# Performance work log

Hardware: AMD Instinct MI355X
Metric: run time of the kernel (lower is better)

## Reference

```python
import jax, jax.numpy as jnp
import numpy as np

L, D, H, DFF = 12, 768, 12, 3072
DH = D // H
EPS = 1e-5


def _layer_norm(x, g, b):
    # manual LN as in source: biased variance, eps inside sqrt
    mean = jnp.mean(x, axis=-1, keepdims=True)
    var = jnp.mean((x - mean) ** 2, axis=-1, keepdims=True)
    return g * (x - mean) / jnp.sqrt(var + EPS) + b


def setup_inputs() -> dict:
    key = jax.random.key(0)
    ks = jax.random.split(key, 10)
    x = jax.random.normal(ks[0], (8, 512, D), dtype=jnp.float32)
    mask = jnp.zeros((8, 1, 1, 512), dtype=jnp.float32)
    s = 0.02
    Wq = jax.random.normal(ks[1], (L, D, D), jnp.float32) * s
    Wk = jax.random.normal(ks[2], (L, D, D), jnp.float32) * s
    Wv = jax.random.normal(ks[3], (L, D, D), jnp.float32) * s
    Wo = jax.random.normal(ks[4], (L, D, D), jnp.float32) * s
    W1 = jax.random.normal(ks[5], (L, DFF, D), jnp.float32) * s
    W2 = jax.random.normal(ks[6], (L, D, DFF), jnp.float32) * s
    z = lambda *sh: jnp.zeros(sh, jnp.float32)
    o = lambda *sh: jnp.ones(sh, jnp.float32)
    return {
        'x': x, 'mask': mask,
        'Wq': Wq, 'bq': z(L, D), 'Wk': Wk, 'bk': z(L, D), 'Wv': Wv, 'bv': z(L, D),
        'Wo': Wo, 'bo': z(L, D), 'g1': o(L, D), 'b1': z(L, D),
        'W1': W1, 'bf1': z(L, DFF), 'W2': W2, 'bf2': z(L, D),
        'g2': o(L, D), 'b2': z(L, D),
    }


def reference(x, mask, Wq, bq, Wk, bk, Wv, bv, Wo, bo, g1, b1, W1, bf1, W2, bf2, g2, b2):
    B, S, _ = x.shape
    scale = 1.0 / jnp.sqrt(jnp.float32(DH))

    def layer(h, p):
        wq, pq, wk, pk, wv, pv, wo, po, gg1, bb1, w1, pf1, w2, pf2, gg2, bb2 = p
        # Dense: x @ W^T + b
        q = (h @ wq.T + pq).reshape(B, S, H, DH).transpose(0, 2, 1, 3)  # [B,H,S,dh]
        k = (h @ wk.T + pk).reshape(B, S, H, DH).transpose(0, 2, 1, 3)
        v = (h @ wv.T + pv).reshape(B, S, H, DH).transpose(0, 2, 1, 3)
        scores = jnp.einsum('bhqd,bhkd->bhqk', q, k) * scale
        scores = scores + mask * -1e9
        attn = jax.nn.softmax(scores, axis=-1)
        ctx = jnp.einsum('bhqk,bhkd->bhqd', attn, v)
        ctx = ctx.transpose(0, 2, 1, 3).reshape(B, S, D)
        a = _layer_norm(h + (ctx @ wo.T + po), gg1, bb1)
        ffn = jnp.maximum(a @ w1.T + pf1, 0.0) @ w2.T + pf2
        out = _layer_norm(a + ffn, gg2, bb2)
        return out, None

    params = (Wq, bq, Wk, bk, Wv, bv, Wo, bo, g1, b1, W1, bf1, W2, bf2, g2, b2)
    out, _ = jax.lax.scan(layer, x, params)
    return out
```

## Files before the change

kernel.cpp:

```cpp
#include <hip/hip_runtime.h>
#include <hip/hip_bf16.h>
#include <stdint.h>

#define DDIM 768
#define NH 12
#define DHD 64
#define DFF 3072
#define NLAYER 12
#define SEQ 512
#define NB 8
#define ROWS (NB*SEQ)

typedef __attribute__((ext_vector_type(4))) float f32x4;
typedef __attribute__((ext_vector_type(8))) short short8;

#define S_BARRIER()  asm volatile("s_barrier" ::: "memory")
#define WAIT_LGKM0() asm volatile("s_waitcnt lgkmcnt(0)" ::: "memory")
#define WAIT_VM0()   asm volatile("s_waitcnt vmcnt(0)" ::: "memory")
#define WAIT_VM3()   asm volatile("s_waitcnt vmcnt(3)" ::: "memory")
#define WAIT_VM4()   asm volatile("s_waitcnt vmcnt(4)" ::: "memory")

static __device__ __forceinline__ short bf16r(float f) {
  union { float f; uint32_t u; } a; a.f = f;
  uint32_t u = a.u;
  u += 0x7FFFu + ((u >> 16) & 1u);
  return (short)(u >> 16);
}

static __device__ __forceinline__ float bf2f(short s) {
  union { uint32_t u; float f; } c;
  c.u = ((uint32_t)(uint16_t)s) << 16;
  return c.f;
}

static __device__ __forceinline__ f32x4 mfma_bf16(short8 a, short8 b, f32x4 c) {
  return __builtin_amdgcn_mfma_f32_16x16x32_bf16(a, b, c, 0, 0, 0);
}

static __device__ __forceinline__ void gload16(const void* g, void* l) {
  __builtin_amdgcn_global_load_lds(
      (__attribute__((address_space(1))) void*)(void*)(uintptr_t)g,
      (__attribute__((address_space(3))) void*)l,
      16, 0, 0);
}

struct WCvt {
  const float* src[4];
  short* dst[4];
  int n8[4];
};

__global__ void wconv_kernel(WCvt wc) {
  const int m = blockIdx.y;
  const float* __restrict__ src = wc.src[m];
  short* __restrict__ dst = wc.dst[m];
  const int n8 = wc.n8[m];
  for (int i = blockIdx.x * 256 + threadIdx.x; i < n8; i += gridDim.x * 256) {
    f32x4 a = *(const f32x4*)(src + (size_t)i * 8);
    f32x4 b = *(const f32x4*)(src + (size_t)i * 8 + 4);
    short8 o;
    o[0] = bf16r(a[0]); o[1] = bf16r(a[1]); o[2] = bf16r(a[2]); o[3] = bf16r(a[3]);
    o[4] = bf16r(b[0]); o[5] = bf16r(b[1]); o[6] = bf16r(b[2]); o[7] = bf16r(b[3]);
    *(short8*)(dst + (size_t)i * 8) = o;
  }
}

struct GemmB {
  const short* W0; const short* W1; const short* W2;
  const float* b0; const float* b1; const float* b2;
  void* o0; void* o1; void* o2;
};

template<int OUTMODE, int BM>
__launch_bounds__(256, 3)
__global__ void gemm_bt(const short* __restrict__ A, GemmB gb, int M, int N, int K) {
  constexpr int MF  = BM / 32;
  constexpr int ISS = BM / 64;

  const int z = blockIdx.z;
  const short* W    = (z == 0) ? gb.W0 : ((z == 1) ? gb.W1 : gb.W2);
  const float* bias = (z == 0) ? gb.b0 : ((z == 1) ? gb.b1 : gb.b2);
  void* outp        = (z == 0) ? gb.o0 : ((z == 1) ? gb.o1 : gb.o2);

  __shared__ __align__(16) short As[2][BM * 32];
  __shared__ __align__(16) short Bs[2][128 * 32];

  const int tid  = threadIdx.x;
  const int lane = tid & 63;
  const int wid  = tid >> 6;
  const int l16  = lane & 15;
  const int kg   = lane >> 4;
  const int wr   = wid >> 1;
  const int wc   = wid & 1;
  const int m0   = blockIdx.x * BM;
  const int n0   = blockIdx.y * 128;

  const f32x4 zero = {0.f, 0.f, 0.f, 0.f};
  f32x4 acc[MF][4];
  #pragma unroll
  for (int i = 0; i < MF; i++)
    #pragma unroll
    for (int j = 0; j < 4; j++) acc[i][j] = zero;

  const int lrow = lane >> 2;
  const int lcol = (lane & 3) * 8;
  const short* Ag = A + (size_t)(m0 + wid * (BM / 4) + lrow) * K + lcol;
  const short* Wg = W + (size_t)(n0 + wid * 32 + lrow) * K + lcol;

  auto stage = [&](int buf, int k0) {
    #pragma unroll
    for (int j = 0; j < ISS; j++)
      gload16(Ag + k0 + (size_t)(j * 16) * K, &As[buf][(wid * (BM / 4) + j * 16) * 32]);
    #pragma unroll
    for (int j = 0; j < 2; j++)
      gload16(Wg + k0 + (size_t)(j * 16) * K, &Bs[buf][(wid * 32 + j * 16) * 32]);
  };

  const int nsteps = K >> 5;
  stage(0, 0);
  stage(1, 32);
  if (ISS == 2) { WAIT_VM4(); } else { WAIT_VM3(); }
  S_BARRIER();

  for (int t = 0; t < nsteps; ++t) {
    const int cur = t & 1;
    short8 af[MF], bfr[4];
    #pragma unroll
    for (int i = 0; i < MF; i++)
      af[i] = *(const short8*)&As[cur][(wr * (BM / 2) + i * 16 + l16) * 32 + kg * 8];
    #pragma unroll
    for (int j = 0; j < 4; j++)
      bfr[j] = *(const short8*)&Bs[cur][(wc * 64 + j * 16 + l16) * 32 + kg * 8];
    WAIT_LGKM0();
    S_BARRIER();

    const bool pf = (t + 2 < nsteps);
    if (pf) stage(cur, (t + 2) << 5);
    __builtin_amdgcn_sched_barrier(0);
    #pragma unroll
    for (int i = 0; i < MF; i++)
      #pragma unroll
      for (int j = 0; j < 4; j++)
        acc[i][j] = mfma_bf16(af[i], bfr[j], acc[i][j]);
    __builtin_amdgcn_sched_barrier(0);

    if (pf) { if (ISS == 2) { WAIT_VM4(); } else { WAIT_VM3(); } }
    else    { WAIT_VM0(); }
    S_BARRIER();
  }

  float* outf = (float*)outp;
  short* outb = (short*)outp;
  #pragma unroll
  for (int j = 0; j < 4; j++) {
    const int col = n0 + wc * 64 + j * 16 + l16;
    const float bv = bias[col];
    #pragma unroll
    for (int i = 0; i < MF; i++) {
      const int row0 = m0 + wr * (BM / 2) + i * 16 + kg * 4;
      #pragma unroll
      for (int e = 0; e < 4; e++) {
        float v = acc[i][j][e] + bv;
        if (OUTMODE == 2) v = fmaxf(v, 0.0f);
        const size_t off = (size_t)(row0 + e) * N + col;
        if (OUTMODE == 0) outf[off] = v;
        else              outb[off] = bf16r(v);
      }
    }
  }
}

__launch_bounds__(256, 2)
__global__ void attn_kernel(const short* __restrict__ Qg, const short* __restrict__ Kg,
                            const short* __restrict__ Vg, const float* __restrict__ mask,
                            short* __restrict__ ctx) {
  __shared__ __align__(16) short Vt[64 * 512];

  const int bh = blockIdx.x;
  const int b = bh / NH;
  const int h = bh % NH;
  const int tid  = threadIdx.x;
  const int lane = tid & 63;
  const int wid  = tid >> 6;
  const int l16  = lane & 15;
  const int kg   = lane >> 4;

  const short* Qb = Qg + (size_t)b * SEQ * DDIM + h * DHD;
  const short* Kb = Kg + (size_t)b * SEQ * DDIM + h * DHD;
  const short* Vb = Vg + (size_t)b * SEQ * DDIM + h * DHD;

  for (int c = tid; c < SEQ * 8; c += 256) {
    const int kv = c >> 3;
    const int d0 = (c & 7) * 8;
    short8 v = *(const short8*)(Vb + (size_t)kv * DDIM + d0);
    #pragma unroll
    for (int j = 0; j < 8; j++)
      Vt[(d0 + j) * 512 + (kv ^ ((j & 3) << 3))] = v[j];
  }
  __syncthreads();

  const int q0 = blockIdx.y * 128 + wid * 32;

  short8 qf[2][2];
  #pragma unroll
  for (int rt = 0; rt < 2; rt++)
    #pragma unroll
    for (int dh = 0; dh < 2; dh++)
      qf[rt][dh] = *(const short8*)(Qb + (size_t)(q0 + rt * 16 + l16) * DDIM + dh * 32 + kg * 8);

  float mrun[2] = {-1e30f, -1e30f};
  float lrun[2] = {0.0f, 0.0f};
  const f32x4 zero = {0.f, 0.f, 0.f, 0.f};
  f32x4 oacc[2][4];
  #pragma unroll
  for (int rt = 0; rt < 2; rt++)
    #pragma unroll
    for (int dt = 0; dt < 4; dt++) oacc[rt][dt] = zero;

  const float* maskb = mask + (size_t)b * SEQ;

  for (int kv0 = 0; kv0 < SEQ; kv0 += 32) {
    short8 kf[2][2];
    #pragma unroll
    for (int kvh = 0; kvh < 2; kvh++)
      #pragma unroll
      for (int dh = 0; dh < 2; dh++)
        kf[kvh][dh] = *(const short8*)(Kb + (size_t)(kv0 + kvh * 16 + l16) * DDIM + dh * 32 + kg * 8);

    short8 vf[4];
    #pragma unroll
    for (int dt = 0; dt < 4; dt++) {
      const int d = dt * 16 + l16;
      vf[dt] = *(const short8*)&Vt[d * 512 + ((kv0 + kg * 8) ^ ((d & 3) << 3))];
    }

    const f32x4 mq0 = *(const f32x4*)(maskb + kv0 + kg * 4);
    const f32x4 mq1 = *(const f32x4*)(maskb + kv0 + 16 + kg * 4);

    #pragma unroll
    for (int rt = 0; rt < 2; rt++) {
      f32x4 s0 = zero, s1 = zero;
      s0 = mfma_bf16(kf[0][0], qf[rt][0], s0);
      s0 = mfma_bf16(kf[0][1], qf[rt][1], s0);
      s1 = mfma_bf16(kf[1][0], qf[rt][0], s1);
      s1 = mfma_bf16(kf[1][1], qf[rt][1], s1);

      float p[8];
      #pragma unroll
      for (int e = 0; e < 4; e++) {
        p[e]     = s0[e] * 0.125f + mq0[e] * (-1e9f);
        p[e + 4] = s1[e] * 0.125f + mq1[e] * (-1e9f);
      }
      float mt = p[0];
      #pragma unroll
      for (int e = 1; e < 8; e++) mt = fmaxf(mt, p[e]);
      mt = fmaxf(mt, __shfl_xor(mt, 16, 64));
      mt = fmaxf(mt, __shfl_xor(mt, 32, 64));
      const float mnew = fmaxf(mrun[rt], mt);
      const float corr = __expf(mrun[rt] - mnew);
      float ts = 0.0f;
      #pragma unroll
      for (int e = 0; e < 8; e++) { p[e] = __expf(p[e] - mnew); ts += p[e]; }
      ts += __shfl_xor(ts, 16, 64);
      ts += __shfl_xor(ts, 32, 64);
      lrun[rt] = lrun[rt] * corr + ts;
      mrun[rt] = mnew;

      const int P0 = (int)(((uint32_t)(uint16_t)bf16r(p[1]) << 16) | (uint16_t)bf16r(p[0]));
      const int P1 = (int)(((uint32_t)(uint16_t)bf16r(p[3]) << 16) | (uint16_t)bf16r(p[2]));
      const int P2 = (int)(((uint32_t)(uint16_t)bf16r(p[5]) << 16) | (uint16_t)bf16r(p[4]));
      const int P3 = (int)(((uint32_t)(uint16_t)bf16r(p[7]) << 16) | (uint16_t)bf16r(p[6]));
      const int sl0 = (((2 * kg) & 3) << 4) + l16;
      const int sl1 = (((2 * kg + 1) & 3) << 4) + l16;
      const int x0 = __shfl(P0, sl0, 64), y0 = __shfl(P2, sl0, 64);
      const int x1 = __shfl(P1, sl0, 64), y1 = __shfl(P3, sl0, 64);
      const int x2 = __shfl(P0, sl1, 64), y2 = __shfl(P2, sl1, 64);
      const int x3 = __shfl(P1, sl1, 64), y3 = __shfl(P3, sl1, 64);
      union { int w[4]; short8 v; } pa;
      const bool hi = (kg >= 2);
      pa.w[0] = hi ? y0 : x0;
      pa.w[1] = hi ? y1 : x1;
      pa.w[2] = hi ? y2 : x2;
      pa.w[3] = hi ? y3 : x3;

      const float c0 = __shfl(corr, kg * 4 + 0, 64);
      const float c1 = __shfl(corr, kg * 4 + 1, 64);
      const float c2 = __shfl(corr, kg * 4 + 2, 64);
      const float c3 = __shfl(corr, kg * 4 + 3, 64);

      #pragma unroll
      for (int dt = 0; dt < 4; dt++) {
        f32x4 o = oacc[rt][dt];
        o[0] *= c0; o[1] *= c1; o[2] *= c2; o[3] *= c3;
        oacc[rt][dt] = mfma_bf16(pa.v, vf[dt], o);
      }
    }
  }

  short* cb = ctx + (size_t)b * SEQ * DDIM + h * DHD;
  #pragma unroll
  for (int rt = 0; rt < 2; rt++) {
    const float li = 1.0f / lrun[rt];
    const float l0 = __shfl(li, kg * 4 + 0, 64);
    const float l1 = __shfl(li, kg * 4 + 1, 64);
    const float l2 = __shfl(li, kg * 4 + 2, 64);
    const float l3 = __shfl(li, kg * 4 + 3, 64);
    #pragma unroll
    for (int dt = 0; dt < 4; dt++) {
      const f32x4 o = oacc[rt][dt];
      const int col = dt * 16 + l16;
      const size_t base = (size_t)(q0 + rt * 16 + kg * 4) * DDIM + col;
      cb[base + 0 * DDIM] = bf16r(o[0] * l0);
      cb[base + 1 * DDIM] = bf16r(o[1] * l1);
      cb[base + 2 * DDIM] = bf16r(o[2] * l2);
      cb[base + 3 * DDIM] = bf16r(o[3] * l3);
    }
  }
}

template<int PBF16>
__launch_bounds__(256, 4)
__global__ void ln_kernel(const float* __restrict__ resid, const void* __restrict__ projv,
                          const float* __restrict__ gw, const float* __restrict__ bw,
                          float* __restrict__ outf, short* __restrict__ outb) {
  const int lane = threadIdx.x & 63;
  const int wid  = threadIdx.x >> 6;
  const int row  = blockIdx.x * 4 + wid;
  const float* rp = resid + (size_t)row * DDIM;
  float v[12];
  float s = 0.0f;
  #pragma unroll
  for (int c = 0; c < 12; c++) {
    float pv;
    if (PBF16) pv = bf2f(((const short*)projv)[(size_t)row * DDIM + c * 64 + lane]);
    else       pv = ((const float*)projv)[(size_t)row * DDIM + c * 64 + lane];
    v[c] = rp[c * 64 + lane] + pv;
    s += v[c];
  }
  #pragma unroll
  for (int o = 1; o < 64; o <<= 1) s += __shfl_xor(s, o, 64);
  const float mean = s * (1.0f / 768.0f);
  float q = 0.0f;
  #pragma unroll
  for (int c = 0; c < 12; c++) { const float d = v[c] - mean; q += d * d; }
  #pragma unroll
  for (int o = 1; o < 64; o <<= 1) q += __shfl_xor(q, o, 64);
  const float inv = 1.0f / sqrtf(q * (1.0f / 768.0f) + 1e-5f);
  #pragma unroll
  for (int c = 0; c < 12; c++) {
    const int idx = c * 64 + lane;
    const float y = gw[idx] * (v[c] - mean) * inv + bw[idx];
    outf[(size_t)row * DDIM + idx] = y;
    outb[(size_t)row * DDIM + idx] = bf16r(y);
  }
}

extern "C" void kernel_launch(void* const* d_in, const int* in_sizes, int n_in,
                              void* d_out, int out_size, void* d_ws, size_t ws_size,
                              hipStream_t stream) {
  const float* x    = (const float*)d_in[0];
  const float* mask = (const float*)d_in[1];
  const float* Wq   = (const float*)d_in[2];
  const float* bq   = (const float*)d_in[3];
  const float* Wk   = (const float*)d_in[4];
  const float* bk   = (const float*)d_in[5];
  const float* Wv   = (const float*)d_in[6];
  const float* bv   = (const float*)d_in[7];
  const float* Wo   = (const float*)d_in[8];
  const float* bo   = (const float*)d_in[9];
  const float* g1   = (const float*)d_in[10];
  const float* b1   = (const float*)d_in[11];
  const float* W1   = (const float*)d_in[12];
  const float* bf1  = (const float*)d_in[13];
  const float* W2   = (const float*)d_in[14];
  const float* bf2  = (const float*)d_in[15];
  const float* g2   = (const float*)d_in[16];
  const float* b2   = (const float*)d_in[17];

  const size_t SD  = (size_t)ROWS * DDIM;
  const size_t WDD = (size_t)DDIM * DDIM;
  const size_t WFD = (size_t)DFF * DDIM;

  char* ws = (char*)d_ws;
  float* H0   = (float*)ws;  ws += SD * 4;
  short* Bbuf = (short*)ws;  ws += SD * 2;
  short* R1   = (short*)ws;  ws += (size_t)ROWS * DFF * 2;
  short* WB   = (short*)ws;

  short* Qb = R1;
  short* Kb = R1 + SD;
  short* Vb = R1 + 2 * SD;
  short* Cb = R1 + 3 * SD;
  float* Pf = (float*)R1;

  {
    WCvt c{};
    c.src[0] = x; c.dst[0] = Bbuf; c.n8[0] = (int)(SD / 8);
    wconv_kernel<<<dim3(1536, 1), 256, 0, stream>>>(c);
  }

  for (int l = 0; l < NLAYER; l++) {
    {
      WCvt c{};
      c.src[0] = Wq + l * WDD; c.dst[0] = WB;           c.n8[0] = (int)(WDD / 8);
      c.src[1] = Wk + l * WDD; c.dst[1] = WB + WDD;     c.n8[1] = (int)(WDD / 8);
      c.src[2] = Wv + l * WDD; c.dst[2] = WB + 2 * WDD; c.n8[2] = (int)(WDD / 8);
      c.src[3] = Wo + l * WDD; c.dst[3] = WB + 3 * WDD; c.n8[3] = (int)(WDD / 8);
      wconv_kernel<<<dim3(288, 4), 256, 0, stream>>>(c);
    }

    {
      GemmB g{};
      g.W0 = WB;           g.b0 = bq + l * DDIM; g.o0 = Qb;
      g.W1 = WB + WDD;     g.b1 = bk + l * DDIM; g.o1 = Kb;
      g.W2 = WB + 2 * WDD; g.b2 = bv + l * DDIM; g.o2 = Vb;
      gemm_bt<1, 128><<<dim3(32, 6, 3), 256, 0, stream>>>(Bbuf, g, ROWS, DDIM, DDIM);
    }

    attn_kernel<<<dim3(NB * NH, 4), 256, 0, stream>>>(Qb, Kb, Vb, mask, Cb);

    {
      GemmB g{};
      g.W0 = WB + 3 * WDD; g.b0 = bo + l * DDIM; g.o0 = Pf;
      gemm_bt<0, 64><<<dim3(64, 6, 1), 256, 0, stream>>>(Cb, g, ROWS, DDIM, DDIM);
    }

    {
      WCvt c{};
      c.src[0] = W1 + l * WFD; c.dst[0] = WB;       c.n8[0] = (int)(WFD / 8);
      c.src[1] = W2 + l * WFD; c.dst[1] = WB + WFD; c.n8[1] = (int)(WFD / 8);
      wconv_kernel<<<dim3(1152, 2), 256, 0, stream>>>(c);
    }

    ln_kernel<0><<<dim3(ROWS / 4), 256, 0, stream>>>(l ? H0 : x, Pf,
                                                     g1 + l * DDIM, b1 + l * DDIM,
                                                     H0, Bbuf);

    {
      GemmB g{};
      g.W0 = WB; g.b0 = bf1 + l * DFF; g.o0 = R1;
      gemm_bt<2, 128><<<dim3(32, 24, 1), 256, 0, stream>>>(Bbuf, g, ROWS, DFF, DDIM);
    }

    {
      GemmB g{};
      g.W0 = WB + WFD; g.b0 = bf2 + l * DDIM; g.o0 = Bbuf;
      gemm_bt<1, 64><<<dim3(64, 6, 1), 256, 0, stream>>>(R1, g, ROWS, DDIM, DFF);
    }

    ln_kernel<1><<<dim3(ROWS / 4), 256, 0, stream>>>(H0, Bbuf,
                                                     g2 + l * DDIM, b2 + l * DDIM,
                                                     (l == NLAYER - 1) ? (float*)d_out : H0,
                                                     Bbuf);
  }
}
```

Before: 2.099 ms.

## Convert all layer weights upfront and fuse QKV into one concatenated GEMM

All twelve layers' weights are converted to bf16 in a single kernel before the layer loop, along with the input, replacing the per-layer conversion launches. Q, K and V weights sit contiguously, so one GEMM with N=2304 and concatenated biases writes an interleaved QKV buffer, which attention now reads with a 2304-element row stride. Separate workspace buffers are used instead of aliasing, and the GEMM launch bound is raised to 4 blocks per CU. This cuts launch count and per-layer conversion traffic, at the cost of a larger workspace and one big upfront conversion pass.

```diff
diff --git a/kernel.cpp b/kernel.cpp
--- a/kernel.cpp
+++ b/kernel.cpp
@@ -10,6 +10,7 @@
 #define SEQ 512
 #define NB 8
 #define ROWS (NB*SEQ)
+#define QS   2304
 
 typedef __attribute__((ext_vector_type(4))) float f32x4;
 typedef __attribute__((ext_vector_type(8))) short short8;
@@ -44,43 +45,67 @@
       16, 0, 0);
 }
 
-struct WCvt {
-  const float* src[4];
-  short* dst[4];
-  int n8[4];
+#define WDD    589824
+#define WFD    2359296
+#define WLAYER (4*WDD + 2*WFD)
+
+struct WAll {
+  const float* src[7];
+  short* wb;
+  short* xb;
 };
 
-__global__ void wconv_kernel(WCvt wc) {
-  const int m = blockIdx.y;
-  const float* __restrict__ src = wc.src[m];
-  short* __restrict__ dst = wc.dst[m];
-  const int n8 = wc.n8[m];
-  for (int i = blockIdx.x * 256 + threadIdx.x; i < n8; i += gridDim.x * 256) {
+__global__ void wconv_all_kernel(WAll wa) {
+  const int y = blockIdx.y;
+  const float* __restrict__ src = wa.src[y];
+  if (y == 6) {
+    short* __restrict__ dst = wa.xb;
+    const int n8 = (ROWS * DDIM) / 8;
+    for (int i = blockIdx.x * 256 + threadIdx.x; i < n8; i += gridDim.x * 256) {
+      f32x4 a = *(const f32x4*)(src + (size_t)i * 8);
+      f32x4 b = *(const f32x4*)(src + (size_t)i * 8 + 4);
+      short8 o;
+      o[0] = bf16r(a[0]); o[1] = bf16r(a[1]); o[2] = bf16r(a[2]); o[3] = bf16r(a[3]);
+      o[4] = bf16r(b[0]); o[5] = bf16r(b[1]); o[6] = bf16r(b[2]); o[7] = bf16r(b[3]);
+      *(short8*)(dst + (size_t)i * 8) = o;
+    }
+    return;
+  }
+  const int perL8  = (y < 4 ? WDD : WFD) / 8;
+  const int dstOff = (y < 4) ? y * WDD : 4 * WDD + (y - 4) * WFD;
+  const int tot    = NLAYER * perL8;
+  for (int i = blockIdx.x * 256 + threadIdx.x; i < tot; i += gridDim.x * 256) {
+    const int l = i / perL8;
+    const int r = i - l * perL8;
     f32x4 a = *(const f32x4*)(src + (size_t)i * 8);
     f32x4 b = *(const f32x4*)(src + (size_t)i * 8 + 4);
     short8 o;
     o[0] = bf16r(a[0]); o[1] = bf16r(a[1]); o[2] = bf16r(a[2]); o[3] = bf16r(a[3]);
     o[4] = bf16r(b[0]); o[5] = bf16r(b[1]); o[6] = bf16r(b[2]); o[7] = bf16r(b[3]);
-    *(short8*)(dst + (size_t)i * 8) = o;
-  }
-}
-
-struct GemmB {
-  const short* W0; const short* W1; const short* W2;
-  const float* b0; const float* b1; const float* b2;
-  void* o0; void* o1; void* o2;
-};
+    *(short8*)(wa.wb + (size_t)l * WLAYER + dstOff + (size_t)r * 8) = o;
+  }
+}
+
+__global__ void bcat_kernel(const float* __restrict__ bq, const float* __restrict__ bk,
+                            const float* __restrict__ bv, float* __restrict__ out) {
+  const int idx = blockIdx.x * 256 + threadIdx.x;
+  if (idx >= NLAYER * QS) return;
+  const int l = idx / QS;
+  const int j = idx - l * QS;
+  float v;
+  if (j < DDIM)            v = bq[l * DDIM + j];
+  else if (j < 2 * DDIM)   v = bk[l * DDIM + j - DDIM];
+  else                     v = bv[l * DDIM + j - 2 * DDIM];
+  out[idx] = v;
+}
 
 template<int OUTMODE, int BM>
-__launch_bounds__(256, 3)
-__global__ void gemm_bt(const short* __restrict__ A, GemmB gb, int M, int N, int K) {
+__launch_bounds__(256, 4)
+__global__ void gemm_bt(const short* __restrict__ A, const short* __restrict__ W,
+                        const float* __restrict__ bias, void* __restrict__ outp,
+                        int M, int N, int K) {
   constexpr int MF  = BM / 32;
   constexpr int ISS = BM / 64;
-
-  const int z = blockIdx.z;
-  const short* W    = (z == 0) ? gb.W0 : ((z == 1) ? gb.W1 : gb.W2);
-  const float* bias = (z == 0) ? gb.b0 : ((z == 1) ? gb.b1 : gb.b2);
-  void* outp        = (z == 0) ? gb.o0 : ((z == 1) ? gb.o1 : gb.o2);
 
   __shared__ __align__(16) short As[2][BM * 32];
   __shared__ __align__(16) short Bs[2][128 * 32];
@@ -171,8 +196,7 @@
 }
 
 __launch_bounds__(256, 2)
-__global__ void attn_kernel(const short* __restrict__ Qg, const short* __restrict__ Kg,
-                            const short* __restrict__ Vg, const float* __restrict__ mask,
+__global__ void attn_kernel(const short* __restrict__ QKV, const float* __restrict__ mask,
                             short* __restrict__ ctx) {
   __shared__ __align__(16) short Vt[64 * 512];
 
@@ -185,14 +209,14 @@
   const int l16  = lane & 15;
   const int kg   = lane >> 4;
 
-  const short* Qb = Qg + (size_t)b * SEQ * DDIM + h * DHD;
-  const short* Kb = Kg + (size_t)b * SEQ * DDIM + h * DHD;
-  const short* Vb = Vg + (size_t)b * SEQ * DDIM + h * DHD;
+  const short* Qb = QKV + (size_t)b * SEQ * QS + h * DHD;
+  const short* Kb = Qb + DDIM;
+  const short* Vb = Qb + 2 * DDIM;
 
   for (int c = tid; c < SEQ * 8; c += 256) {
     const int kv = c >> 3;
     const int d0 = (c & 7) * 8;
-    short8 v = *(const short8*)(Vb + (size_t)kv * DDIM + d0);
+    short8 v = *(const short8*)(Vb + (size_t)kv * QS + d0);
     #pragma unroll
     for (int j = 0; j < 8; j++)
       Vt[(d0 + j) * 512 + (kv ^ ((j & 3) << 3))] = v[j];
@@ -206,7 +230,7 @@
   for (int rt = 0; rt < 2; rt++)
     #pragma unroll
     for (int dh = 0; dh < 2; dh++)
-      qf[rt][dh] = *(const short8*)(Qb + (size_t)(q0 + rt * 16 + l16) * DDIM + dh * 32 + kg * 8);
+      qf[rt][dh] = *(const short8*)(Qb + (size_t)(q0 + rt * 16 + l16) * QS + dh * 32 + kg * 8);
 
   float mrun[2] = {-1e30f, -1e30f};
   float lrun[2] = {0.0f, 0.0f};
@@ -225,7 +249,7 @@
     for (int kvh = 0; kvh < 2; kvh++)
       #pragma unroll
       for (int dh = 0; dh < 2; dh++)
-        kf[kvh][dh] = *(const short8*)(Kb + (size_t)(kv0 + kvh * 16 + l16) * DDIM + dh * 32 + kg * 8);
+        kf[kvh][dh] = *(const short8*)(Kb + (size_t)(kv0 + kvh * 16 + l16) * QS + dh * 32 + kg * 8);
 
     short8 vf[4];
     #pragma unroll
@@ -377,79 +401,50 @@
   const float* g2   = (const float*)d_in[16];
   const float* b2   = (const float*)d_in[17];
 
-  const size_t SD  = (size_t)ROWS * DDIM;
-  const size_t WDD = (size_t)DDIM * DDIM;
-  const size_t WFD = (size_t)DFF * DDIM;
+  const size_t SD = (size_t)ROWS * DDIM;
 
   char* ws = (char*)d_ws;
   float* H0   = (float*)ws;  ws += SD * 4;
   short* Bbuf = (short*)ws;  ws += SD * 2;
-  short* R1   = (short*)ws;  ws += (size_t)ROWS * DFF * 2;
+  short* QKVb = (short*)ws;  ws += (size_t)ROWS * QS * 2;
+  short* Cb   = (short*)ws;  ws += SD * 2;
+  float* Pf   = (float*)ws;  ws += SD * 4;
+  short* F1   = (short*)ws;  ws += (size_t)ROWS * DFF * 2;
+  float* Bqkv = (float*)ws;  ws += (size_t)NLAYER * QS * 4;
   short* WB   = (short*)ws;
 
-  short* Qb = R1;
-  short* Kb = R1 + SD;
-  short* Vb = R1 + 2 * SD;
-  short* Cb = R1 + 3 * SD;
-  float* Pf = (float*)R1;
-
   {
-    WCvt c{};
-    c.src[0] = x; c.dst[0] = Bbuf; c.n8[0] = (int)(SD / 8);
-    wconv_kernel<<<dim3(1536, 1), 256, 0, stream>>>(c);
+    WAll wa{};
+    wa.src[0] = Wq; wa.src[1] = Wk; wa.src[2] = Wv; wa.src[3] = Wo;
+    wa.src[4] = W1; wa.src[5] = W2; wa.src[6] = x;
+    wa.wb = WB; wa.xb = Bbuf;
+    wconv_all_kernel<<<dim3(1024, 7), 256, 0, stream>>>(wa);
+    bcat_kernel<<<dim3((NLAYER * QS + 255) / 256), 256, 0, stream>>>(bq, bk, bv, Bqkv);
   }
 
   for (int l = 0; l < NLAYER; l++) {
-    {
-      WCvt c{};
-      c.src[0] = Wq + l * WDD; c.dst[0] = WB;           c.n8[0] = (int)(WDD / 8);
-      c.src[1] = Wk + l * WDD; c.dst[1] = WB + WDD;     c.n8[1] = (int)(WDD / 8);
-      c.src[2] = Wv + l * WDD; c.dst[2] = WB + 2 * WDD; c.n8[2] = (int)(WDD / 8);
-      c.src[3] = Wo + l * WDD; c.dst[3] = WB + 3 * WDD; c.n8[3] = (int)(WDD / 8);
-      wconv_kernel<<<dim3(288, 4), 256, 0, stream>>>(c);
-    }
-
-    {
-      GemmB g{};
-      g.W0 = WB;           g.b0 = bq + l * DDIM; g.o0 = Qb;
-      g.W1 = WB + WDD;     g.b1 = bk + l * DDIM; g.o1 = Kb;
-      g.W2 = WB + 2 * WDD; g.b2 = bv + l * DDIM; g.o2 = Vb;
-      gemm_bt<1, 128><<<dim3(32, 6, 3), 256, 0, stream>>>(Bbuf, g, ROWS, DDIM, DDIM);
-    }
-
-    attn_kernel<<<dim3(NB * NH, 4), 256, 0, stream>>>(Qb, Kb, Vb, mask, Cb);
-
-    {
-      GemmB g{};
-      g.W0 = WB + 3 * WDD; g.b0 = bo + l * DDIM; g.o0 = Pf;
-      gemm_bt<0, 64><<<dim3(64, 6, 1), 256, 0, stream>>>(Cb, g, ROWS, DDIM, DDIM);
-    }
-
-    {
-      WCvt c{};
-      c.src[0] = W1 + l * WFD; c.dst[0] = WB;       c.n8[0] = (int)(WFD / 8);
-      c.src[1] = W2 + l * WFD; c.dst[1] = WB + WFD; c.n8[1] = (int)(WFD / 8);
-      wconv_kernel<<<dim3(1152, 2), 256, 0, stream>>>(c);
-    }
+    const short* WL = WB + (size_t)l * WLAYER;
+
+    gemm_bt<1, 128><<<dim3(32, 18), 256, 0, stream>>>(
+        Bbuf, WL, Bqkv + (size_t)l * QS, QKVb, ROWS, QS, DDIM);
+
+    attn_kernel<<<dim3(NB * NH, 4), 256, 0, stream>>>(QKVb, mask, Cb);
+
+    gemm_bt<0, 64><<<dim3(64, 6), 256, 0, stream>>>(
+        Cb, WL + 3 * WDD, bo + (size_t)l * DDIM, Pf, ROWS, DDIM, DDIM);
 
     ln_kernel<0><<<dim3(ROWS / 4), 256, 0, stream>>>(l ? H0 : x, Pf,
-                                                     g1 + l * DDIM, b1 + l * DDIM,
+                                                     g1 + (size_t)l * DDIM, b1 + (size_t)l * DDIM,
                                                      H0, Bbuf);
 
-    {
-      GemmB g{};
-      g.W0 = WB; g.b0 = bf1 + l * DFF; g.o0 = R1;
-      gemm_bt<2, 128><<<dim3(32, 24, 1), 256, 0, stream>>>(Bbuf, g, ROWS, DFF, DDIM);
-    }
-
-    {
-      GemmB g{};
-      g.W0 = WB + WFD; g.b0 = bf2 + l * DDIM; g.o0 = Bbuf;
-      gemm_bt<1, 64><<<dim3(64, 6, 1), 256, 0, stream>>>(R1, g, ROWS, DDIM, DFF);
-    }
+    gemm_bt<2, 128><<<dim3(32, 24), 256, 0, stream>>>(
+        Bbuf, WL + 4 * WDD, bf1 + (size_t)l * DFF, F1, ROWS, DFF, DDIM);
+
+    gemm_bt<1, 64><<<dim3(64, 6), 256, 0, stream>>>(
+        F1, WL + 4 * WDD + WFD, bf2 + (size_t)l * DDIM, Bbuf, ROWS, DDIM, DFF);
 
     ln_kernel<1><<<dim3(ROWS / 4), 256, 0, stream>>>(H0, Bbuf,
-                                                     g2 + l * DDIM, b2 + l * DDIM,
+                                                     g2 + (size_t)l * DDIM, b2 + (size_t)l * DDIM,
                                                      (l == NLAYER - 1) ? (float*)d_out : H0,
                                                      Bbuf);
   }
```

Measured after the change: 2.238 ms. 1.07x slower.

## Fuse next-layer weight bf16 conversion into FFN1 GEMM with double-buffered weights

Applied to the files above, without the earlier changes.

Removes the two per-layer weight-conversion launches. The FFN1 GEMM grid gets 9 extra rows of blocks (288 blocks) that convert the next layer's attention and FFN weights into a second, ping-pong weight buffer while the GEMM tiles run. This saves launches and lets the memory-bound conversion overlap the compute-bound GEMM. The cost is a double workspace for bf16 weights and possible contention between the converter blocks and the GEMM blocks for bandwidth and CU slots.

```diff
diff --git a/kernel.cpp b/kernel.cpp
--- a/kernel.cpp
+++ b/kernel.cpp
@@ -20,6 +20,9 @@
 #define WAIT_VM3()   asm volatile("s_waitcnt vmcnt(3)" ::: "memory")
 #define WAIT_VM4()   asm volatile("s_waitcnt vmcnt(4)" ::: "memory")
 
+#define WDD    589824
+#define WFD    2359296
+
 static __device__ __forceinline__ short bf16r(float f) {
   union { float f; uint32_t u; } a; a.f = f;
   uint32_t u = a.u;
@@ -44,6 +47,16 @@
       16, 0, 0);
 }
 
+static __device__ __forceinline__ void cvt8(const float* __restrict__ s,
+                                            short* __restrict__ d) {
+  f32x4 a = *(const f32x4*)(s);
+  f32x4 b = *(const f32x4*)(s + 4);
+  short8 o;
+  o[0] = bf16r(a[0]); o[1] = bf16r(a[1]); o[2] = bf16r(a[2]); o[3] = bf16r(a[3]);
+  o[4] = bf16r(b[0]); o[5] = bf16r(b[1]); o[6] = bf16r(b[2]); o[7] = bf16r(b[3]);
+  *(short8*)d = o;
+}
+
 struct WCvt {
   const float* src[4];
   short* dst[4];
@@ -55,14 +68,8 @@
   const float* __restrict__ src = wc.src[m];
   short* __restrict__ dst = wc.dst[m];
   const int n8 = wc.n8[m];
-  for (int i = blockIdx.x * 256 + threadIdx.x; i < n8; i += gridDim.x * 256) {
-    f32x4 a = *(const f32x4*)(src + (size_t)i * 8);
-    f32x4 b = *(const f32x4*)(src + (size_t)i * 8 + 4);
-    short8 o;
-    o[0] = bf16r(a[0]); o[1] = bf16r(a[1]); o[2] = bf16r(a[2]); o[3] = bf16r(a[3]);
-    o[4] = bf16r(b[0]); o[5] = bf16r(b[1]); o[6] = bf16r(b[2]); o[7] = bf16r(b[3]);
-    *(short8*)(dst + (size_t)i * 8) = o;
-  }
+  for (int i = blockIdx.x * 256 + threadIdx.x; i < n8; i += gridDim.x * 256)
+    cvt8(src + (size_t)i * 8, dst + (size_t)i * 8);
 }
 
 struct GemmB {
@@ -71,11 +78,36 @@
   void* o0; void* o1; void* o2;
 };
 
-template<int OUTMODE, int BM>
+struct ConvNext {
+  const float* srcA[4];
+  const float* srcB[2];
+  short* dstA;
+  short* dstB;
+};
+
+template<int OUTMODE, int BM, int FUSECONV>
 __launch_bounds__(256, 3)
-__global__ void gemm_bt(const short* __restrict__ A, GemmB gb, int M, int N, int K) {
+__global__ void gemm_bt(const short* __restrict__ A, GemmB gb, ConvNext cn,
+                        int M, int N, int K, int nby) {
   constexpr int MF  = BM / 32;
   constexpr int ISS = BM / 64;
+
+  if (FUSECONV && (int)blockIdx.y >= nby) {
+    const int cid = ((int)blockIdx.y - nby) * (int)gridDim.x + (int)blockIdx.x;
+    for (int i = cid * 256 + (int)threadIdx.x; i < 884736; i += 288 * 256) {
+      if (i < 294912) {
+        const int m = i / 73728;
+        const int r = i - m * 73728;
+        cvt8(cn.srcA[m] + (size_t)r * 8, cn.dstA + (size_t)m * WDD + (size_t)r * 8);
+      } else {
+        const int c2 = i - 294912;
+        const int m = c2 / 294912;
+        const int r = c2 - m * 294912;
+        cvt8(cn.srcB[m] + (size_t)r * 8, cn.dstB + (size_t)m * WFD + (size_t)r * 8);
+      }
+    }
+    return;
+  }
 
   const int z = blockIdx.z;
   const short* W    = (z == 0) ? gb.W0 : ((z == 1) ? gb.W1 : gb.W2);
@@ -377,15 +409,18 @@
   const float* g2   = (const float*)d_in[16];
   const float* b2   = (const float*)d_in[17];
 
-  const size_t SD  = (size_t)ROWS * DDIM;
-  const size_t WDD = (size_t)DDIM * DDIM;
-  const size_t WFD = (size_t)DFF * DDIM;
+  const size_t SD = (size_t)ROWS * DDIM;
 
   char* ws = (char*)d_ws;
-  float* H0   = (float*)ws;  ws += SD * 4;
-  short* Bbuf = (short*)ws;  ws += SD * 2;
-  short* R1   = (short*)ws;  ws += (size_t)ROWS * DFF * 2;
-  short* WB   = (short*)ws;
+  float* H0     = (float*)ws;  ws += SD * 4;
+  short* Bbuf   = (short*)ws;  ws += SD * 2;
+  short* R1     = (short*)ws;  ws += (size_t)ROWS * DFF * 2;
+  short* WBa[2];
+  WBa[0] = (short*)ws;  ws += (size_t)4 * WDD * 2;
+  WBa[1] = (short*)ws;  ws += (size_t)4 * WDD * 2;
+  short* WBb[2];
+  WBb[0] = (short*)ws;  ws += (size_t)2 * WFD * 2;
+  WBb[1] = (short*)ws;  ws += (size_t)2 * WFD * 2;
 
   short* Qb = R1;
   short* Kb = R1 + SD;
@@ -398,58 +433,76 @@
     c.src[0] = x; c.dst[0] = Bbuf; c.n8[0] = (int)(SD / 8);
     wconv_kernel<<<dim3(1536, 1), 256, 0, stream>>>(c);
   }
+  {
+    WCvt c{};
+    c.src[0] = Wq; c.dst[0] = WBa[0];           c.n8[0] = (int)(WDD / 8);
+    c.src[1] = Wk; c.dst[1] = WBa[0] + WDD;     c.n8[1] = (int)(WDD / 8);
+    c.src[2] = Wv; c.dst[2] = WBa[0] + 2 * WDD; c.n8[2] = (int)(WDD / 8);
+    c.src[3] = Wo; c.dst[3] = WBa[0] + 3 * WDD; c.n8[3] = (int)(WDD / 8);
+    wconv_kernel<<<dim3(288, 4), 256, 0, stream>>>(c);
+  }
+  {
+    WCvt c{};
+    c.src[0] = W1; c.dst[0] = WBb[0];       c.n8[0] = (int)(WFD / 8);
+    c.src[1] = W2; c.dst[1] = WBb[0] + WFD; c.n8[1] = (int)(WFD / 8);
+    wconv_kernel<<<dim3(1152, 2), 256, 0, stream>>>(c);
+  }
+
+  const ConvNext cnDummy{};
 
   for (int l = 0; l < NLAYER; l++) {
-    {
-      WCvt c{};
-      c.src[0] = Wq + l * WDD; c.dst[0] = WB;           c.n8[0] = (int)(WDD / 8);
-      c.src[1] = Wk + l * WDD; c.dst[1] = WB + WDD;     c.n8[1] = (int)(WDD / 8);
-      c.src[2] = Wv + l * WDD; c.dst[2] = WB + 2 * WDD; c.n8[2] = (int)(WDD / 8);
-      c.src[3] = Wo + l * WDD; c.dst[3] = WB + 3 * WDD; c.n8[3] = (int)(WDD / 8);
-      wconv_kernel<<<dim3(288, 4), 256, 0, stream>>>(c);
-    }
+    const short* WA = WBa[l & 1];
+    const short* WF = WBb[l & 1];
 
     {
       GemmB g{};
-      g.W0 = WB;           g.b0 = bq + l * DDIM; g.o0 = Qb;
-      g.W1 = WB + WDD;     g.b1 = bk + l * DDIM; g.o1 = Kb;
-      g.W2 = WB + 2 * WDD; g.b2 = bv + l * DDIM; g.o2 = Vb;
-      gemm_bt<1, 128><<<dim3(32, 6, 3), 256, 0, stream>>>(Bbuf, g, ROWS, DDIM, DDIM);
+      g.W0 = WA;           g.b0 = bq + (size_t)l * DDIM; g.o0 = Qb;
+      g.W1 = WA + WDD;     g.b1 = bk + (size_t)l * DDIM; g.o1 = Kb;
+      g.W2 = WA + 2 * WDD; g.b2 = bv + (size_t)l * DDIM; g.o2 = Vb;
+      gemm_bt<1, 128, 0><<<dim3(32, 6, 3), 256, 0, stream>>>(
+          Bbuf, g, cnDummy, ROWS, DDIM, DDIM, 6);
     }
 
     attn_kernel<<<dim3(NB * NH, 4), 256, 0, stream>>>(Qb, Kb, Vb, mask, Cb);
 
     {
       GemmB g{};
-      g.W0 = WB + 3 * WDD; g.b0 = bo + l * DDIM; g.o0 = Pf;
-      gemm_bt<0, 64><<<dim3(64, 6, 1), 256, 0, stream>>>(Cb, g, ROWS, DDIM, DDIM);
-    }
-
-    {
-      WCvt c{};
-      c.src[0] = W1 + l * WFD; c.dst[0] = WB;       c.n8[0] = (int)(WFD / 8);
-      c.src[1] = W2 + l * WFD; c.dst[1] = WB + WFD; c.n8[1] = (int)(WFD / 8);
-      wconv_kernel<<<dim3(1152, 2), 256, 0, stream>>>(c);
+      g.W0 = WA + 3 * WDD; g.b0 = bo + (size_t)l * DDIM; g.o0 = Pf;
+      gemm_bt<0, 64, 0><<<dim3(64, 6, 1), 256, 0, stream>>>(
+          Cb, g, cnDummy, ROWS, DDIM, DDIM, 6);
     }
 
     ln_kernel<0><<<dim3(ROWS / 4), 256, 0, stream>>>(l ? H0 : x, Pf,
-                                                     g1 + l * DDIM, b1 + l * DDIM,
+                                                     g1 + (size_t)l * DDIM, b1 + (size_t)l * DDIM,
                                                      H0, Bbuf);
 
     {
       GemmB g{};
-      g.W0 = WB; g.b0 = bf1 + l * DFF; g.o0 = R1;
-      gemm_bt<2, 128><<<dim3(32, 24, 1), 256, 0, stream>>>(Bbuf, g, ROWS, DFF, DDIM);
+      g.W0 = WF; g.b0 = bf1 + (size_t)l * DFF; g.o0 = R1;
+      const int nl = (l + 1 < NLAYER) ? (l + 1) : l;
+      ConvNext cn{};
+      cn.srcA[0] = Wq + (size_t)nl * WDD;
+      cn.srcA[1] = Wk + (size_t)nl * WDD;
+      cn.srcA[2] = Wv + (size_t)nl * WDD;
+      cn.srcA[3] = Wo + (size_t)nl * WDD;
+      cn.srcB[0] = W1 + (size_t)nl * WFD;
+      cn.srcB[1] = W2 + (size_t)nl * WFD;
+      cn.dstA = WBa[(l + 1) & 1];
+      cn.dstB = WBb[(l + 1) & 1];
+      const int gy = (l + 1 < NLAYER) ? 33 : 24;
+      gemm_bt<2, 128, 1><<<dim3(32, gy, 1), 256, 0, stream>>>(
+          Bbuf, g, cn, ROWS, DFF, DDIM, 24);
     }
 
     {
       GemmB g{};
-      g.W0 = WB + WFD; g.b0 = bf2 + l * DDIM; g.o0 = Bbuf;
-      gemm_bt<1, 64><<<dim3(64, 6, 1), 256, 0, stream>>>(R1, g, ROWS, DDIM, DFF);
+      g.W0 = WF + WFD; g.b0 = bf2 + (size_t)l * DDIM; g.o0 = Bbuf;
+      gemm_bt<1, 64, 0><<<dim3(64, 6, 1), 256, 0, stream>>>(
+          R1, g, cnDummy, ROWS, DDIM, DFF, 6);
     }
 
     ln_kernel<1><<<dim3(ROWS / 4), 256, 0, stream>>>(H0, Bbuf,
-                                                     g2 + l * DDIM, b2 + l * DDIM,
+                                                     g2 + (size_t)l * DDIM, b2 + (size_t)l * DDIM,
                                                      (l == NLAYER - 1) ? (float*)d_out : H0,
                                                      Bbuf);
   }
```

Measured after the change: 2.154 ms. +2.6%, slower.

## Split-K the N=768 projection GEMMs and fuse partial reduction into LayerNorm

Applied to the files above, without the earlier changes.

The Wo and W2 GEMMs (N=768, grid 64x6=384 blocks) now run as 2-way split-K, doubling the block count to raise occupancy across the CUs. Each half writes fp32 partial sums to separate workspace buffers, and a new LayerNorm kernel adds residual, both partials and bias before normalising. The cost is extra fp32 partial traffic (two 12 MB buffers written and read) and a larger workspace. The FFN2 output also changes from bf16 to fp32 partials, which slightly alters precision.

```diff
diff --git a/kernel.cpp b/kernel.cpp
--- a/kernel.cpp
+++ b/kernel.cpp
@@ -19,6 +19,9 @@
 #define WAIT_VM0()   asm volatile("s_waitcnt vmcnt(0)" ::: "memory")
 #define WAIT_VM3()   asm volatile("s_waitcnt vmcnt(3)" ::: "memory")
 #define WAIT_VM4()   asm volatile("s_waitcnt vmcnt(4)" ::: "memory")
+
+#define WDD    589824
+#define WFD    2359296
 
 static __device__ __forceinline__ short bf16r(float f) {
   union { float f; uint32_t u; } a; a.f = f;
@@ -71,16 +74,26 @@
   void* o0; void* o1; void* o2;
 };
 
-template<int OUTMODE, int BM>
+template<int OUTMODE, int BM, int SPLITK>
 __launch_bounds__(256, 3)
-__global__ void gemm_bt(const short* __restrict__ A, GemmB gb, int M, int N, int K) {
+__global__ void gemm_bt(const short* __restrict__ A, GemmB gb,
+                        int M, int N, int Kstride, int Klen) {
   constexpr int MF  = BM / 32;
   constexpr int ISS = BM / 64;
 
   const int z = blockIdx.z;
-  const short* W    = (z == 0) ? gb.W0 : ((z == 1) ? gb.W1 : gb.W2);
-  const float* bias = (z == 0) ? gb.b0 : ((z == 1) ? gb.b1 : gb.b2);
-  void* outp        = (z == 0) ? gb.o0 : ((z == 1) ? gb.o1 : gb.o2);
+  const short* W;
+  const float* bias;
+  void* outp;
+  if (SPLITK) {
+    W    = gb.W0 + (size_t)z * Klen;
+    bias = gb.b0;
+    outp = (z == 0) ? gb.o0 : gb.o1;
+  } else {
+    W    = (z == 0) ? gb.W0 : ((z == 1) ? gb.W1 : gb.W2);
+    bias = (z == 0) ? gb.b0 : ((z == 1) ? gb.b1 : gb.b2);
+    outp = (z == 0) ? gb.o0 : ((z == 1) ? gb.o1 : gb.o2);
+  }
 
   __shared__ __align__(16) short As[2][BM * 32];
   __shared__ __align__(16) short Bs[2][128 * 32];
@@ -104,19 +117,20 @@
 
   const int lrow = lane >> 2;
   const int lcol = (lane & 3) * 8;
-  const short* Ag = A + (size_t)(m0 + wid * (BM / 4) + lrow) * K + lcol;
-  const short* Wg = W + (size_t)(n0 + wid * 32 + lrow) * K + lcol;
+  const short* Ag = A + (size_t)(m0 + wid * (BM / 4) + lrow) * Kstride + lcol
+                      + (SPLITK ? (size_t)z * Klen : 0);
+  const short* Wg = W + (size_t)(n0 + wid * 32 + lrow) * Kstride + lcol;
 
   auto stage = [&](int buf, int k0) {
     #pragma unroll
     for (int j = 0; j < ISS; j++)
-      gload16(Ag + k0 + (size_t)(j * 16) * K, &As[buf][(wid * (BM / 4) + j * 16) * 32]);
+      gload16(Ag + k0 + (size_t)(j * 16) * Kstride, &As[buf][(wid * (BM / 4) + j * 16) * 32]);
     #pragma unroll
     for (int j = 0; j < 2; j++)
-      gload16(Wg + k0 + (size_t)(j * 16) * K, &Bs[buf][(wid * 32 + j * 16) * 32]);
+      gload16(Wg + k0 + (size_t)(j * 16) * Kstride, &Bs[buf][(wid * 32 + j * 16) * 32]);
   };
 
-  const int nsteps = K >> 5;
+  const int nsteps = Klen >> 5;
   stage(0, 0);
   stage(1, 32);
   if (ISS == 2) { WAIT_VM4(); } else { WAIT_VM3(); }
@@ -154,7 +168,7 @@
   #pragma unroll
   for (int j = 0; j < 4; j++) {
     const int col = n0 + wc * 64 + j * 16 + l16;
-    const float bv = bias[col];
+    const float bv = (OUTMODE == 3) ? 0.0f : bias[col];
     #pragma unroll
     for (int i = 0; i < MF; i++) {
       const int row0 = m0 + wr * (BM / 2) + i * 16 + kg * 4;
@@ -163,7 +177,7 @@
         float v = acc[i][j][e] + bv;
         if (OUTMODE == 2) v = fmaxf(v, 0.0f);
         const size_t off = (size_t)(row0 + e) * N + col;
-        if (OUTMODE == 0) outf[off] = v;
+        if (OUTMODE == 3) outf[off] = v;
         else              outb[off] = bf16r(v);
       }
     }
@@ -318,23 +332,24 @@
   }
 }
 
-template<int PBF16>
 __launch_bounds__(256, 4)
-__global__ void ln_kernel(const float* __restrict__ resid, const void* __restrict__ projv,
-                          const float* __restrict__ gw, const float* __restrict__ bw,
-                          float* __restrict__ outf, short* __restrict__ outb) {
+__global__ void ln_red_kernel(const float* __restrict__ resid,
+                              const float* __restrict__ p0,
+                              const float* __restrict__ p1,
+                              const float* __restrict__ pb,
+                              const float* __restrict__ gw,
+                              const float* __restrict__ bw,
+                              float* __restrict__ outf, short* __restrict__ outb) {
   const int lane = threadIdx.x & 63;
   const int wid  = threadIdx.x >> 6;
   const int row  = blockIdx.x * 4 + wid;
-  const float* rp = resid + (size_t)row * DDIM;
+  const size_t base = (size_t)row * DDIM;
   float v[12];
   float s = 0.0f;
   #pragma unroll
   for (int c = 0; c < 12; c++) {
-    float pv;
-    if (PBF16) pv = bf2f(((const short*)projv)[(size_t)row * DDIM + c * 64 + lane]);
-    else       pv = ((const float*)projv)[(size_t)row * DDIM + c * 64 + lane];
-    v[c] = rp[c * 64 + lane] + pv;
+    const int idx = c * 64 + lane;
+    v[c] = resid[base + idx] + p0[base + idx] + p1[base + idx] + pb[idx];
     s += v[c];
   }
   #pragma unroll
@@ -350,8 +365,8 @@
   for (int c = 0; c < 12; c++) {
     const int idx = c * 64 + lane;
     const float y = gw[idx] * (v[c] - mean) * inv + bw[idx];
-    outf[(size_t)row * DDIM + idx] = y;
-    outb[(size_t)row * DDIM + idx] = bf16r(y);
+    outf[base + idx] = y;
+    outb[base + idx] = bf16r(y);
   }
 }
 
@@ -377,21 +392,20 @@
   const float* g2   = (const float*)d_in[16];
   const float* b2   = (const float*)d_in[17];
 
-  const size_t SD  = (size_t)ROWS * DDIM;
-  const size_t WDD = (size_t)DDIM * DDIM;
-  const size_t WFD = (size_t)DFF * DDIM;
+  const size_t SD = (size_t)ROWS * DDIM;
 
   char* ws = (char*)d_ws;
   float* H0   = (float*)ws;  ws += SD * 4;
   short* Bbuf = (short*)ws;  ws += SD * 2;
   short* R1   = (short*)ws;  ws += (size_t)ROWS * DFF * 2;
-  short* WB   = (short*)ws;
+  short* WB   = (short*)ws;  ws += (size_t)2 * WFD * 2;
+  float* P0   = (float*)ws;  ws += SD * 4;
+  float* P1   = (float*)ws;
 
   short* Qb = R1;
   short* Kb = R1 + SD;
   short* Vb = R1 + 2 * SD;
   short* Cb = R1 + 3 * SD;
-  float* Pf = (float*)R1;
 
   {
     WCvt c{};
@@ -402,55 +416,57 @@
   for (int l = 0; l < NLAYER; l++) {
     {
       WCvt c{};
-      c.src[0] = Wq + l * WDD; c.dst[0] = WB;           c.n8[0] = (int)(WDD / 8);
-      c.src[1] = Wk + l * WDD; c.dst[1] = WB + WDD;     c.n8[1] = (int)(WDD / 8);
-      c.src[2] = Wv + l * WDD; c.dst[2] = WB + 2 * WDD; c.n8[2] = (int)(WDD / 8);
-      c.src[3] = Wo + l * WDD; c.dst[3] = WB + 3 * WDD; c.n8[3] = (int)(WDD / 8);
+      c.src[0] = Wq + (size_t)l * WDD; c.dst[0] = WB;           c.n8[0] = (int)(WDD / 8);
+      c.src[1] = Wk + (size_t)l * WDD; c.dst[1] = WB + WDD;     c.n8[1] = (int)(WDD / 8);
+      c.src[2] = Wv + (size_t)l * WDD; c.dst[2] = WB + 2 * WDD; c.n8[2] = (int)(WDD / 8);
+      c.src[3] = Wo + (size_t)l * WDD; c.dst[3] = WB + 3 * WDD; c.n8[3] = (int)(WDD / 8);
       wconv_kernel<<<dim3(288, 4), 256, 0, stream>>>(c);
     }
 
     {
       GemmB g{};
-      g.W0 = WB;           g.b0 = bq + l * DDIM; g.o0 = Qb;
-      g.W1 = WB + WDD;     g.b1 = bk + l * DDIM; g.o1 = Kb;
-      g.W2 = WB + 2 * WDD; g.b2 = bv + l * DDIM; g.o2 = Vb;
-      gemm_bt<1, 128><<<dim3(32, 6, 3), 256, 0, stream>>>(Bbuf, g, ROWS, DDIM, DDIM);
+      g.W0 = WB;           g.b0 = bq + (size_t)l * DDIM; g.o0 = Qb;
+      g.W1 = WB + WDD;     g.b1 = bk + (size_t)l * DDIM; g.o1 = Kb;
+      g.W2 = WB + 2 * WDD; g.b2 = bv + (size_t)l * DDIM; g.o2 = Vb;
+      gemm_bt<1, 128, 0><<<dim3(32, 6, 3), 256, 0, stream>>>(Bbuf, g, ROWS, DDIM, DDIM, DDIM);
     }
 
     attn_kernel<<<dim3(NB * NH, 4), 256, 0, stream>>>(Qb, Kb, Vb, mask, Cb);
 
     {
       GemmB g{};
-      g.W0 = WB + 3 * WDD; g.b0 = bo + l * DDIM; g.o0 = Pf;
-      gemm_bt<0, 64><<<dim3(64, 6, 1), 256, 0, stream>>>(Cb, g, ROWS, DDIM, DDIM);
-    }
+      g.W0 = WB + 3 * WDD; g.b0 = bo; g.o0 = P0; g.o1 = P1;
+      gemm_bt<3, 64, 1><<<dim3(64, 6, 2), 256, 0, stream>>>(Cb, g, ROWS, DDIM, DDIM, DDIM / 2);
+    }
+
+    ln_red_kernel<<<dim3(ROWS / 4), 256, 0, stream>>>(l ? H0 : x, P0, P1,
+                                                      bo + (size_t)l * DDIM,
+                                                      g1 + (size_t)l * DDIM, b1 + (size_t)l * DDIM,
+                                                      H0, Bbuf);
 
     {
       WCvt c{};
-      c.src[0] = W1 + l * WFD; c.dst[0] = WB;       c.n8[0] = (int)(WFD / 8);
-      c.src[1] = W2 + l * WFD; c.dst[1] = WB + WFD; c.n8[1] = (int)(WFD / 8);
+      c.src[0] = W1 + (size_t)l * WFD; c.dst[0] = WB;       c.n8[0] = (int)(WFD / 8);
+      c.src[1] = W2 + (size_t)l * WFD; c.dst[1] = WB + WFD; c.n8[1] = (int)(WFD / 8);
       wconv_kernel<<<dim3(1152, 2), 256, 0, stream>>>(c);
     }
 
-    ln_kernel<0><<<dim3(ROWS / 4), 256, 0, stream>>>(l ? H0 : x, Pf,
-                                                     g1 + l * DDIM, b1 + l * DDIM,
-                                                     H0, Bbuf);
-
     {
       GemmB g{};
-      g.W0 = WB; g.b0 = bf1 + l * DFF; g.o0 = R1;
-      gemm_bt<2, 128><<<dim3(32, 24, 1), 256, 0, stream>>>(Bbuf, g, ROWS, DFF, DDIM);
+      g.W0 = WB; g.b0 = bf1 + (size_t)l * DFF; g.o0 = R1;
+      gemm_bt<2, 128, 0><<<dim3(32, 24, 1), 256, 0, stream>>>(Bbuf, g, ROWS, DFF, DDIM, DDIM);
     }
 
     {
       GemmB g{};
-      g.W0 = WB + WFD; g.b0 = bf2 + l * DDIM; g.o0 = Bbuf;
-      gemm_bt<1, 64><<<dim3(64, 6, 1), 256, 0, stream>>>(R1, g, ROWS, DDIM, DFF);
-    }
-
-    ln_kernel<1><<<dim3(ROWS / 4), 256, 0, stream>>>(H0, Bbuf,
-                                                     g2 + l * DDIM, b2 + l * DDIM,
-                                                     (l == NLAYER - 1) ? (float*)d_out : H0,
-                                                     Bbuf);
-  }
-}
+      g.W0 = WB + WFD; g.b0 = bf2; g.o0 = P0; g.o1 = P1;
+      gemm_bt<3, 64, 1><<<dim3(64, 6, 2), 256, 0, stream>>>(R1, g, ROWS, DDIM, DFF, DFF / 2);
+    }
+
+    ln_red_kernel<<<dim3(ROWS / 4), 256, 0, stream>>>(H0, P0, P1,
+                                                      bf2 + (size_t)l * DDIM,
+                                                      g2 + (size_t)l * DDIM, b2 + (size_t)l * DDIM,
+                                                      (l == NLAYER - 1) ? (float*)d_out : H0,
+                                                      Bbuf);
+  }
+}
```

Result: faster. 1.968 ms, median of 2 (-6.2%).
